# Kernel optimization log

Hardware: AMD Instinct MI355X
Metric: run time of the kernel (lower is better)

## Reference

```python
import jax, jax.numpy as jnp
import numpy as np

D_MODEL = 768
MIMO_RANK = 4


def setup_inputs() -> dict:
    key = jax.random.key(0)
    ks = jax.random.split(key, 6)
    B, T, D, R = 2, 2048, D_MODEL, MIMO_RANK
    x = jax.random.normal(ks[0], (B, T, D), dtype=jnp.float32)
    norm_w = jnp.ones((D,), dtype=jnp.float32)
    W_in = jax.random.normal(ks[1], (D * R * 2, D), dtype=jnp.float32) * 0.02
    W_out = jax.random.normal(ks[2], (D, D), dtype=jnp.float32) * 0.02
    a_param = jax.random.normal(ks[3], (D, R, 2), dtype=jnp.float32) * 0.12
    b_param = jax.random.normal(ks[4], (D, R, 2), dtype=jnp.float32) * 0.15
    c_param = jax.random.normal(ks[5], (D, R, 2), dtype=jnp.float32) * 0.15
    return {"x": x, "norm_w": norm_w, "W_in": W_in, "W_out": W_out,
            "a_param": a_param, "b_param": b_param, "c_param": c_param}


def reference(x, norm_w, W_in, W_out, a_param, b_param, c_param):
    B, T, D = x.shape
    R = a_param.shape[1]
    # RMSNorm
    xn = x * jax.lax.rsqrt(jnp.mean(x * x, axis=-1, keepdims=True) + 1e-6) * norm_w
    # in_proj -> interleaved complex MIMO input u: [B,T,D,R,2]
    u = (xn @ W_in.T).reshape(B, T, D, R, 2)
    # coefficients (tanh-bounded; |a| scaled by 0.97 for stability)
    a = jnp.tanh(a_param) * 0.97
    b = jnp.tanh(b_param)
    c = jnp.tanh(c_param)
    ac = jax.lax.complex(a[..., 0], a[..., 1])  # [D,R]
    bc = jax.lax.complex(b[..., 0], b[..., 1])
    cc = jax.lax.complex(c[..., 0], c[..., 1])
    uc = jax.lax.complex(u[..., 0], u[..., 1])  # [B,T,D,R]
    # linear complex recurrence s_t = a * s_{t-1} + b * u_t, zero init state,
    # parallelized with an associative scan over time.
    bu = bc[None, None] * uc
    A = jnp.broadcast_to(ac[None, None], bu.shape)

    def comb(l, r):
        return (l[0] * r[0], r[0] * l[1] + r[1])

    _, s = jax.lax.associative_scan(comb, (A, bu), axis=1)  # [B,T,D,R] complex
    # output mix: real part of c * h, summed over MIMO rank -> [B,T,D]
    y = jnp.real(cc[None, None] * s).sum(axis=-1)
    return y @ W_out.T
```

## Files before the change

kernel.cpp:

```cpp
#include <hip/hip_runtime.h>
#include <hip/hip_bf16.h>
#include <stdint.h>

#define BATCH 2
#define TT 2048
#define DM 768
#define RR 4
#define M_TOK 4096
#define NFEAT 6144
#define NCH 6144
#define CHUNK 64
#define NCHUNK 32

typedef __attribute__((ext_vector_type(8))) short short8;
typedef __attribute__((ext_vector_type(4))) float float4v;

__device__ inline float bf2f(uint32_t bits16) {
    union { uint32_t u; float f; } x; x.u = bits16 << 16; return x.f;
}

typedef const __attribute__((address_space(1))) void* gptr_t;
typedef __attribute__((address_space(3))) void* lptr_t;

__device__ inline void async_ld16(const void* g, void* l) {
    __builtin_amdgcn_global_load_lds((gptr_t)(uintptr_t)g, (lptr_t)(uintptr_t)l,
                                     16, 0, 0);
}

__device__ inline void store_c(__hip_bfloat16* C, size_t idx, float v) {
    C[idx] = __float2bfloat16(v);
}
__device__ inline void store_c(float* C, size_t idx, float v) { C[idx] = v; }

__global__ void prep_kernel(const float* __restrict__ W_in,
                            const float* __restrict__ W_out,
                            const float* __restrict__ ap,
                            const float* __restrict__ bp,
                            const float* __restrict__ cp,
                            __hip_bfloat16* __restrict__ Win_bf,
                            __hip_bfloat16* __restrict__ Wout_bf,
                            float2* __restrict__ ac, float2* __restrict__ bc,
                            float2* __restrict__ cc, float2* __restrict__ aL) {
    const int n1 = NFEAT * DM;
    const int n2 = DM * DM;
    int i = blockIdx.x * 256 + threadIdx.x;
    if (i < n1) Win_bf[i] = __float2bfloat16(W_in[i]);
    else if (i < n1 + n2) Wout_bf[i - n1] = __float2bfloat16(W_out[i - n1]);
    if (i < DM * RR) {
        float ar = tanhf(ap[2 * i])     * 0.97f;
        float ai = tanhf(ap[2 * i + 1]) * 0.97f;
        ac[i] = make_float2(ar, ai);
        bc[i] = make_float2(tanhf(bp[2 * i]), tanhf(bp[2 * i + 1]));
        cc[i] = make_float2(tanhf(cp[2 * i]), tanhf(cp[2 * i + 1]));
        float xr = ar, xi = ai;
        #pragma unroll
        for (int k = 0; k < 6; ++k) {
            float nr = xr * xr - xi * xi;
            float ni = 2.f * xr * xi;
            xr = nr; xi = ni;
        }
        aL[i] = make_float2(xr, xi);
    }
}

__global__ __launch_bounds__(256) void rmsnorm_kernel(
    const float* __restrict__ x, const float* __restrict__ w,
    __hip_bfloat16* __restrict__ xn) {
    int row = blockIdx.x;
    const float* xr = x + (size_t)row * DM;
    int tid = threadIdx.x;
    float v0 = xr[tid], v1 = xr[tid + 256], v2 = xr[tid + 512];
    float ss = v0 * v0 + v1 * v1 + v2 * v2;
    #pragma unroll
    for (int o = 1; o < 64; o <<= 1) ss += __shfl_xor(ss, o);
    __shared__ float wsum[4];
    if ((tid & 63) == 0) wsum[tid >> 6] = ss;
    __syncthreads();
    float tot = wsum[0] + wsum[1] + wsum[2] + wsum[3];
    float scale = rsqrtf(tot * (1.f / DM) + 1e-6f);
    size_t base = (size_t)row * DM;
    xn[base + tid]       = __float2bfloat16(v0 * scale * w[tid]);
    xn[base + tid + 256] = __float2bfloat16(v1 * scale * w[tid + 256]);
    xn[base + tid + 512] = __float2bfloat16(v2 * scale * w[tid + 512]);
}

template <int BM, int BN, typename OutT>
__global__ __launch_bounds__(256) void gemm_bt(
    const __hip_bfloat16* __restrict__ A, const __hip_bfloat16* __restrict__ B,
    OutT* __restrict__ C, int M, int N, int K) {
    constexpr int MI = BM / 32;
    constexpr int NJ = BN / 32;
    __shared__ __attribute__((aligned(16))) __hip_bfloat16 lA[BM * 64];
    __shared__ __attribute__((aligned(16))) __hip_bfloat16 lB[BN * 64];
    const int tid  = threadIdx.x;
    const int lane = tid & 63;
    const int wave = tid >> 6;
    const int quad = lane >> 4;
    const int l15  = lane & 15;
    const int wm = (wave >> 1) * (BM / 2);
    const int wn = (wave & 1) * (BN / 2);
    const int m0 = blockIdx.y * BM;
    const int n0 = blockIdx.x * BN;

    float4v acc[MI][NJ] = {};

    for (int k0 = 0; k0 < K; k0 += 64) {
        __syncthreads();
        #pragma unroll
        for (int it = 0; it < BM / 32; ++it) {
            int p = it * 256 + tid;
            int row = p >> 3;
            int cg = (p & 7) ^ (row & 7);
            async_ld16(A + (size_t)(m0 + row) * K + k0 + cg * 8, lA + p * 8);
        }
        #pragma unroll
        for (int it = 0; it < BN / 32; ++it) {
            int p = it * 256 + tid;
            int row = p >> 3;
            int cg = (p & 7) ^ (row & 7);
            async_ld16(B + (size_t)(n0 + row) * K + k0 + cg * 8, lB + p * 8);
        }
        __syncthreads();
        #pragma unroll
        for (int s = 0; s < 2; ++s) {
            short8 af[MI], bfr[NJ];
            #pragma unroll
            for (int i = 0; i < MI; ++i) {
                int r = wm + i * 16 + l15;
                int c = (s * 4 + quad) ^ (r & 7);
                af[i] = *(const short8*)(lA + r * 64 + c * 8);
            }
            #pragma unroll
            for (int j = 0; j < NJ; ++j) {
                int r = wn + j * 16 + l15;
                int c = (s * 4 + quad) ^ (r & 7);
                bfr[j] = *(const short8*)(lB + r * 64 + c * 8);
            }
            #pragma unroll
            for (int i = 0; i < MI; ++i)
                #pragma unroll
                for (int j = 0; j < NJ; ++j)
                    acc[i][j] = __builtin_amdgcn_mfma_f32_16x16x32_bf16(
                        af[i], bfr[j], acc[i][j], 0, 0, 0);
        }
    }
    #pragma unroll
    for (int i = 0; i < MI; ++i)
        #pragma unroll
        for (int j = 0; j < NJ; ++j)
            #pragma unroll
            for (int rg = 0; rg < 4; ++rg) {
                int row = m0 + wm + i * 16 + quad * 4 + rg;
                int col = n0 + wn + j * 16 + l15;
                store_c(C, (size_t)row * N + col, acc[i][j][rg]);
            }
}

__global__ __launch_bounds__(256) void scan_passA(
    const uint32_t* __restrict__ u,
    const float2* __restrict__ ac, const float2* __restrict__ bc,
    float2* __restrict__ chunkEnd) {
    int c = blockIdx.x * 256 + threadIdx.x;
    int j = blockIdx.y;
    int b = c >= DM * RR;
    int rem = c - b * DM * RR;
    float2 a = ac[rem], bb = bc[rem];
    float sr = 0.f, si = 0.f;
    size_t base = ((size_t)b * TT + (size_t)j * CHUNK) * (DM * RR) + rem;
    #pragma unroll 8
    for (int i = 0; i < CHUNK; ++i) {
        uint32_t uw = u[base + (size_t)i * (DM * RR)];
        float ur = bf2f(uw & 0xffffu), ui = bf2f(uw >> 16);
        float tr = bb.x * ur - bb.y * ui;
        float ti = bb.x * ui + bb.y * ur;
        float nr = a.x * sr - a.y * si + tr;
        float ni = a.x * si + a.y * sr + ti;
        sr = nr; si = ni;
    }
    chunkEnd[(size_t)j * NCH + c] = make_float2(sr, si);
}

__global__ __launch_bounds__(256) void scan_passC(
    const uint32_t* __restrict__ u,
    const float2* __restrict__ ac, const float2* __restrict__ bc,
    const float2* __restrict__ cc, const float2* __restrict__ aLp,
    const float2* __restrict__ chunkEnd,
    __hip_bfloat16* __restrict__ y) {
    int c = blockIdx.x * 256 + threadIdx.x;
    int j = blockIdx.y;
    int b = c >= DM * RR;
    int rem = c - b * DM * RR;
    int d = rem >> 2;
    float2 a = ac[rem], bb = bc[rem], cf = cc[rem];
    float2 aL = aLp[rem];
    float sr = 0.f, si = 0.f;
    #pragma unroll 4
    for (int jj = 0; jj < j; ++jj) {
        float2 e = chunkEnd[(size_t)jj * NCH + c];
        float nr = aL.x * sr - aL.y * si + e.x;
        float ni = aL.x * si + aL.y * sr + e.y;
        sr = nr; si = ni;
    }
    size_t ubase = ((size_t)b * TT + (size_t)j * CHUNK) * (DM * RR) + rem;
    size_t ybase = ((size_t)b * TT + (size_t)j * CHUNK) * DM + d;
    #pragma unroll 4
    for (int i = 0; i < CHUNK; ++i) {
        uint32_t uw = u[ubase + (size_t)i * (DM * RR)];
        float ur = bf2f(uw & 0xffffu), ui = bf2f(uw >> 16);
        float tr = bb.x * ur - bb.y * ui;
        float ti = bb.x * ui + bb.y * ur;
        float nr = a.x * sr - a.y * si + tr;
        float ni = a.x * si + a.y * sr + ti;
        sr = nr; si = ni;
        float contrib = cf.x * sr - cf.y * si;
        contrib += __shfl_xor(contrib, 1);
        contrib += __shfl_xor(contrib, 2);
        if ((threadIdx.x & 3) == 0)
            y[ybase + (size_t)i * DM] = __float2bfloat16(contrib);
    }
}

extern "C" void kernel_launch(void* const* d_in, const int* in_sizes, int n_in,
                              void* d_out, int out_size, void* d_ws,
                              size_t ws_size, hipStream_t stream) {
    const float* x      = (const float*)d_in[0];
    const float* norm_w = (const float*)d_in[1];
    const float* W_in   = (const float*)d_in[2];
    const float* W_out  = (const float*)d_in[3];
    const float* a_p    = (const float*)d_in[4];
    const float* b_p    = (const float*)d_in[5];
    const float* c_p    = (const float*)d_in[6];
    float* out = (float*)d_out;

    char* ws = (char*)d_ws;
    size_t off = 0;
    auto alloc = [&](size_t bytes) {
        void* p = ws + off;
        off += (bytes + 255) & ~(size_t)255;
        return p;
    };
    __hip_bfloat16* Win_bf  = (__hip_bfloat16*)alloc((size_t)NFEAT * DM * 2);
    __hip_bfloat16* Wout_bf = (__hip_bfloat16*)alloc((size_t)DM * DM * 2);
    __hip_bfloat16* xn      = (__hip_bfloat16*)alloc((size_t)M_TOK * DM * 2);
    __hip_bfloat16* u       = (__hip_bfloat16*)alloc((size_t)M_TOK * NFEAT * 2);
    __hip_bfloat16* y       = (__hip_bfloat16*)alloc((size_t)M_TOK * DM * 2);
    float2* ac = (float2*)alloc((size_t)DM * RR * 8);
    float2* bc = (float2*)alloc((size_t)DM * RR * 8);
    float2* cc = (float2*)alloc((size_t)DM * RR * 8);
    float2* aL = (float2*)alloc((size_t)DM * RR * 8);
    float2* chunkEnd = (float2*)alloc((size_t)NCHUNK * NCH * 8);

    {
        int n_total = NFEAT * DM + DM * DM;
        prep_kernel<<<(n_total + 255) / 256, 256, 0, stream>>>(
            W_in, W_out, a_p, b_p, c_p, Win_bf, Wout_bf, ac, bc, cc, aL);
    }
    rmsnorm_kernel<<<M_TOK, 256, 0, stream>>>(x, norm_w, xn);
    gemm_bt<128, 128, __hip_bfloat16>
        <<<dim3(NFEAT / 128, M_TOK / 128), 256, 0, stream>>>(
            xn, Win_bf, u, M_TOK, NFEAT, DM);
    scan_passA<<<dim3(NCH / 256, NCHUNK), 256, 0, stream>>>(
        (const uint32_t*)u, ac, bc, chunkEnd);
    scan_passC<<<dim3(NCH / 256, NCHUNK), 256, 0, stream>>>(
        (const uint32_t*)u, ac, bc, cc, aL, chunkEnd, y);
    gemm_bt<64, 64, float>
        <<<dim3(DM / 64, M_TOK / 64), 256, 0, stream>>>(
            y, Wout_bf, out, M_TOK, DM, DM);
}
```

Baseline: 192.7 us.

## Vectorize prep/rmsnorm, per-channel scan with rank-4 threads, add carry pass, BK=128 out-GEMM

The weight conversion and RMSNorm now use float4 loads and packed bf16 stores. The scan kernels assign one thread per model channel, handling all four MIMO ranks through a single 16-byte load, which removes the shuffle reduction in the output pass. A new passB computes the inter-chunk carries once, replacing the per-block serial prefix that every passC block used to recompute. The output GEMM uses a BK of 128. In exchange there is one extra kernel launch and a carry buffer, and the scan now launches 4x fewer threads, which lowers parallelism.

```diff
diff --git a/kernel.cpp b/kernel.cpp
--- a/kernel.cpp
+++ b/kernel.cpp
@@ -32,20 +32,31 @@
 }
 __device__ inline void store_c(float* C, size_t idx, float v) { C[idx] = v; }
 
-__global__ void prep_kernel(const float* __restrict__ W_in,
-                            const float* __restrict__ W_out,
-                            const float* __restrict__ ap,
-                            const float* __restrict__ bp,
-                            const float* __restrict__ cp,
-                            __hip_bfloat16* __restrict__ Win_bf,
-                            __hip_bfloat16* __restrict__ Wout_bf,
-                            float2* __restrict__ ac, float2* __restrict__ bc,
-                            float2* __restrict__ cc, float2* __restrict__ aL) {
-    const int n1 = NFEAT * DM;
-    const int n2 = DM * DM;
+__device__ inline uint2 pack4bf(float a, float b, float c, float d) {
+    union { __hip_bfloat16 h[4]; uint2 u; } o;
+    o.h[0] = __float2bfloat16(a); o.h[1] = __float2bfloat16(b);
+    o.h[2] = __float2bfloat16(c); o.h[3] = __float2bfloat16(d);
+    return o.u;
+}
+
+__global__ __launch_bounds__(256) void prep_kernel(
+    const float* __restrict__ W_in, const float* __restrict__ W_out,
+    const float* __restrict__ ap, const float* __restrict__ bp,
+    const float* __restrict__ cp,
+    __hip_bfloat16* __restrict__ Win_bf, __hip_bfloat16* __restrict__ Wout_bf,
+    float2* __restrict__ ac, float2* __restrict__ bc,
+    float2* __restrict__ cc, float2* __restrict__ aL) {
+    const int N1 = NFEAT * DM / 4;
+    const int N2 = DM * DM / 4;
     int i = blockIdx.x * 256 + threadIdx.x;
-    if (i < n1) Win_bf[i] = __float2bfloat16(W_in[i]);
-    else if (i < n1 + n2) Wout_bf[i - n1] = __float2bfloat16(W_out[i - n1]);
+    if (i < N1) {
+        float4 v = ((const float4*)W_in)[i];
+        ((uint2*)Win_bf)[i] = pack4bf(v.x, v.y, v.z, v.w);
+    } else if (i < N1 + N2) {
+        int k = i - N1;
+        float4 v = ((const float4*)W_out)[k];
+        ((uint2*)Wout_bf)[k] = pack4bf(v.x, v.y, v.z, v.w);
+    }
     if (i < DM * RR) {
         float ar = tanhf(ap[2 * i])     * 0.97f;
         float ai = tanhf(ap[2 * i + 1]) * 0.97f;
@@ -63,35 +74,35 @@
     }
 }
 
-__global__ __launch_bounds__(256) void rmsnorm_kernel(
+__global__ __launch_bounds__(192) void rmsnorm_kernel(
     const float* __restrict__ x, const float* __restrict__ w,
     __hip_bfloat16* __restrict__ xn) {
     int row = blockIdx.x;
-    const float* xr = x + (size_t)row * DM;
     int tid = threadIdx.x;
-    float v0 = xr[tid], v1 = xr[tid + 256], v2 = xr[tid + 512];
-    float ss = v0 * v0 + v1 * v1 + v2 * v2;
+    float4 v = ((const float4*)(x + (size_t)row * DM))[tid];
+    float ss = v.x * v.x + v.y * v.y + v.z * v.z + v.w * v.w;
     #pragma unroll
     for (int o = 1; o < 64; o <<= 1) ss += __shfl_xor(ss, o);
-    __shared__ float wsum[4];
+    __shared__ float wsum[3];
     if ((tid & 63) == 0) wsum[tid >> 6] = ss;
     __syncthreads();
-    float tot = wsum[0] + wsum[1] + wsum[2] + wsum[3];
+    float tot = wsum[0] + wsum[1] + wsum[2];
     float scale = rsqrtf(tot * (1.f / DM) + 1e-6f);
-    size_t base = (size_t)row * DM;
-    xn[base + tid]       = __float2bfloat16(v0 * scale * w[tid]);
-    xn[base + tid + 256] = __float2bfloat16(v1 * scale * w[tid + 256]);
-    xn[base + tid + 512] = __float2bfloat16(v2 * scale * w[tid + 512]);
-}
-
-template <int BM, int BN, typename OutT>
-__global__ __launch_bounds__(256) void gemm_bt(
+    float4 wv = ((const float4*)w)[tid];
+    ((uint2*)(xn + (size_t)row * DM))[tid] =
+        pack4bf(v.x * scale * wv.x, v.y * scale * wv.y,
+                v.z * scale * wv.z, v.w * scale * wv.w);
+}
+
+template <int BM, int BN, int BK, typename OutT>
+__device__ inline void gemm_body(
     const __hip_bfloat16* __restrict__ A, const __hip_bfloat16* __restrict__ B,
     OutT* __restrict__ C, int M, int N, int K) {
     constexpr int MI = BM / 32;
     constexpr int NJ = BN / 32;
-    __shared__ __attribute__((aligned(16))) __hip_bfloat16 lA[BM * 64];
-    __shared__ __attribute__((aligned(16))) __hip_bfloat16 lB[BN * 64];
+    constexpr int CPR = BK / 8;
+    __shared__ __attribute__((aligned(16))) __hip_bfloat16 lA[BM * BK];
+    __shared__ __attribute__((aligned(16))) __hip_bfloat16 lB[BN * BK];
     const int tid  = threadIdx.x;
     const int lane = tid & 63;
     const int wave = tid >> 6;
@@ -104,37 +115,37 @@
 
     float4v acc[MI][NJ] = {};
 
-    for (int k0 = 0; k0 < K; k0 += 64) {
+    for (int k0 = 0; k0 < K; k0 += BK) {
         __syncthreads();
         #pragma unroll
-        for (int it = 0; it < BM / 32; ++it) {
+        for (int it = 0; it < BM * CPR / 256; ++it) {
             int p = it * 256 + tid;
-            int row = p >> 3;
-            int cg = (p & 7) ^ (row & 7);
+            int row = p / CPR;
+            int cg = (p & (CPR - 1)) ^ (row & (CPR - 1));
             async_ld16(A + (size_t)(m0 + row) * K + k0 + cg * 8, lA + p * 8);
         }
         #pragma unroll
-        for (int it = 0; it < BN / 32; ++it) {
+        for (int it = 0; it < BN * CPR / 256; ++it) {
             int p = it * 256 + tid;
-            int row = p >> 3;
-            int cg = (p & 7) ^ (row & 7);
+            int row = p / CPR;
+            int cg = (p & (CPR - 1)) ^ (row & (CPR - 1));
             async_ld16(B + (size_t)(n0 + row) * K + k0 + cg * 8, lB + p * 8);
         }
         __syncthreads();
         #pragma unroll
-        for (int s = 0; s < 2; ++s) {
+        for (int s = 0; s < BK / 32; ++s) {
             short8 af[MI], bfr[NJ];
             #pragma unroll
             for (int i = 0; i < MI; ++i) {
                 int r = wm + i * 16 + l15;
-                int c = (s * 4 + quad) ^ (r & 7);
-                af[i] = *(const short8*)(lA + r * 64 + c * 8);
+                int c = (s * 4 + quad) ^ (r & (CPR - 1));
+                af[i] = *(const short8*)(lA + r * BK + c * 8);
             }
             #pragma unroll
             for (int j = 0; j < NJ; ++j) {
                 int r = wn + j * 16 + l15;
-                int c = (s * 4 + quad) ^ (r & 7);
-                bfr[j] = *(const short8*)(lB + r * 64 + c * 8);
+                int c = (s * 4 + quad) ^ (r & (CPR - 1));
+                bfr[j] = *(const short8*)(lB + r * BK + c * 8);
             }
             #pragma unroll
             for (int i = 0; i < MI; ++i)
@@ -156,67 +167,102 @@
             }
 }
 
+__global__ __launch_bounds__(256) void gemm_in(
+    const __hip_bfloat16* __restrict__ A, const __hip_bfloat16* __restrict__ B,
+    __hip_bfloat16* __restrict__ C, int M, int N, int K) {
+    gemm_body<128, 128, 64, __hip_bfloat16>(A, B, C, M, N, K);
+}
+
+__global__ __launch_bounds__(256) void gemm_out(
+    const __hip_bfloat16* __restrict__ A, const __hip_bfloat16* __restrict__ B,
+    float* __restrict__ C, int M, int N, int K) {
+    gemm_body<64, 64, 128, float>(A, B, C, M, N, K);
+}
+
+__device__ inline void cstep(float& sr, float& si, float2 a, float2 bb,
+                             uint32_t uw) {
+    float ur = bf2f(uw & 0xffffu), ui = bf2f(uw >> 16);
+    float tr = bb.x * ur - bb.y * ui;
+    float ti = bb.x * ui + bb.y * ur;
+    float nr = a.x * sr - a.y * si + tr;
+    float ni = a.x * si + a.y * sr + ti;
+    sr = nr; si = ni;
+}
+
 __global__ __launch_bounds__(256) void scan_passA(
-    const uint32_t* __restrict__ u,
+    const uint4* __restrict__ u4,
     const float2* __restrict__ ac, const float2* __restrict__ bc,
     float2* __restrict__ chunkEnd) {
+    int g = blockIdx.x * 256 + threadIdx.x;
+    int j = blockIdx.y;
+    int b = g >= DM;
+    int d = g - b * DM;
+    int cb = d * RR;
+    float2 a0 = ac[cb], a1 = ac[cb + 1], a2 = ac[cb + 2], a3 = ac[cb + 3];
+    float2 b0 = bc[cb], b1 = bc[cb + 1], b2 = bc[cb + 2], b3 = bc[cb + 3];
+    float s0r = 0, s0i = 0, s1r = 0, s1i = 0;
+    float s2r = 0, s2i = 0, s3r = 0, s3i = 0;
+    size_t base = ((size_t)(b * TT + j * CHUNK)) * DM + d;
+    #pragma unroll 4
+    for (int i = 0; i < CHUNK; ++i) {
+        uint4 uw = u4[base + (size_t)i * DM];
+        cstep(s0r, s0i, a0, b0, uw.x);
+        cstep(s1r, s1i, a1, b1, uw.y);
+        cstep(s2r, s2i, a2, b2, uw.z);
+        cstep(s3r, s3i, a3, b3, uw.w);
+    }
+    size_t eb = (size_t)j * NCH + b * (DM * RR) + cb;
+    chunkEnd[eb]     = make_float2(s0r, s0i);
+    chunkEnd[eb + 1] = make_float2(s1r, s1i);
+    chunkEnd[eb + 2] = make_float2(s2r, s2i);
+    chunkEnd[eb + 3] = make_float2(s3r, s3i);
+}
+
+__global__ __launch_bounds__(256) void scan_passB(
+    const float2* __restrict__ chunkEnd, const float2* __restrict__ aLp,
+    float2* __restrict__ carry) {
     int c = blockIdx.x * 256 + threadIdx.x;
-    int j = blockIdx.y;
-    int b = c >= DM * RR;
-    int rem = c - b * DM * RR;
-    float2 a = ac[rem], bb = bc[rem];
-    float sr = 0.f, si = 0.f;
-    size_t base = ((size_t)b * TT + (size_t)j * CHUNK) * (DM * RR) + rem;
-    #pragma unroll 8
-    for (int i = 0; i < CHUNK; ++i) {
-        uint32_t uw = u[base + (size_t)i * (DM * RR)];
-        float ur = bf2f(uw & 0xffffu), ui = bf2f(uw >> 16);
-        float tr = bb.x * ur - bb.y * ui;
-        float ti = bb.x * ui + bb.y * ur;
-        float nr = a.x * sr - a.y * si + tr;
-        float ni = a.x * si + a.y * sr + ti;
-        sr = nr; si = ni;
-    }
-    chunkEnd[(size_t)j * NCH + c] = make_float2(sr, si);
-}
-
-__global__ __launch_bounds__(256) void scan_passC(
-    const uint32_t* __restrict__ u,
-    const float2* __restrict__ ac, const float2* __restrict__ bc,
-    const float2* __restrict__ cc, const float2* __restrict__ aLp,
-    const float2* __restrict__ chunkEnd,
-    __hip_bfloat16* __restrict__ y) {
-    int c = blockIdx.x * 256 + threadIdx.x;
-    int j = blockIdx.y;
-    int b = c >= DM * RR;
-    int rem = c - b * DM * RR;
-    int d = rem >> 2;
-    float2 a = ac[rem], bb = bc[rem], cf = cc[rem];
+    int rem = (c >= DM * RR) ? c - DM * RR : c;
     float2 aL = aLp[rem];
     float sr = 0.f, si = 0.f;
-    #pragma unroll 4
-    for (int jj = 0; jj < j; ++jj) {
-        float2 e = chunkEnd[(size_t)jj * NCH + c];
+    for (int j = 0; j < NCHUNK; ++j) {
+        carry[(size_t)j * NCH + c] = make_float2(sr, si);
+        float2 e = chunkEnd[(size_t)j * NCH + c];
         float nr = aL.x * sr - aL.y * si + e.x;
         float ni = aL.x * si + aL.y * sr + e.y;
         sr = nr; si = ni;
     }
-    size_t ubase = ((size_t)b * TT + (size_t)j * CHUNK) * (DM * RR) + rem;
-    size_t ybase = ((size_t)b * TT + (size_t)j * CHUNK) * DM + d;
+}
+
+__global__ __launch_bounds__(256) void scan_passC(
+    const uint4* __restrict__ u4,
+    const float2* __restrict__ ac, const float2* __restrict__ bc,
+    const float2* __restrict__ cc, const float2* __restrict__ carry,
+    __hip_bfloat16* __restrict__ y) {
+    int g = blockIdx.x * 256 + threadIdx.x;
+    int j = blockIdx.y;
+    int b = g >= DM;
+    int d = g - b * DM;
+    int cb = d * RR;
+    float2 a0 = ac[cb], a1 = ac[cb + 1], a2 = ac[cb + 2], a3 = ac[cb + 3];
+    float2 b0 = bc[cb], b1 = bc[cb + 1], b2 = bc[cb + 2], b3 = bc[cb + 3];
+    float2 c0 = cc[cb], c1 = cc[cb + 1], c2 = cc[cb + 2], c3 = cc[cb + 3];
+    size_t kb = (size_t)j * NCH + b * (DM * RR) + cb;
+    float2 k0 = carry[kb], k1 = carry[kb + 1];
+    float2 k2 = carry[kb + 2], k3 = carry[kb + 3];
+    float s0r = k0.x, s0i = k0.y, s1r = k1.x, s1i = k1.y;
+    float s2r = k2.x, s2i = k2.y, s3r = k3.x, s3i = k3.y;
+    size_t base  = ((size_t)(b * TT + j * CHUNK)) * DM + d;
     #pragma unroll 4
     for (int i = 0; i < CHUNK; ++i) {
-        uint32_t uw = u[ubase + (size_t)i * (DM * RR)];
-        float ur = bf2f(uw & 0xffffu), ui = bf2f(uw >> 16);
-        float tr = bb.x * ur - bb.y * ui;
-        float ti = bb.x * ui + bb.y * ur;
-        float nr = a.x * sr - a.y * si + tr;
-        float ni = a.x * si + a.y * sr + ti;
-        sr = nr; si = ni;
-        float contrib = cf.x * sr - cf.y * si;
-        contrib += __shfl_xor(contrib, 1);
-        contrib += __shfl_xor(contrib, 2);
-        if ((threadIdx.x & 3) == 0)
-            y[ybase + (size_t)i * DM] = __float2bfloat16(contrib);
+        uint4 uw = u4[base + (size_t)i * DM];
+        cstep(s0r, s0i, a0, b0, uw.x);
+        cstep(s1r, s1i, a1, b1, uw.y);
+        cstep(s2r, s2i, a2, b2, uw.z);
+        cstep(s3r, s3i, a3, b3, uw.w);
+        float yv = c0.x * s0r - c0.y * s0i + c1.x * s1r - c1.y * s1i
+                 + c2.x * s2r - c2.y * s2i + c3.x * s3r - c3.y * s3i;
+        y[base + (size_t)i * DM] = __float2bfloat16(yv);
     }
 }
 
@@ -249,21 +295,21 @@
     float2* cc = (float2*)alloc((size_t)DM * RR * 8);
     float2* aL = (float2*)alloc((size_t)DM * RR * 8);
     float2* chunkEnd = (float2*)alloc((size_t)NCHUNK * NCH * 8);
+    float2* carry    = (float2*)alloc((size_t)NCHUNK * NCH * 8);
 
     {
-        int n_total = NFEAT * DM + DM * DM;
+        int n_total = (NFEAT * DM + DM * DM) / 4;
         prep_kernel<<<(n_total + 255) / 256, 256, 0, stream>>>(
             W_in, W_out, a_p, b_p, c_p, Win_bf, Wout_bf, ac, bc, cc, aL);
     }
-    rmsnorm_kernel<<<M_TOK, 256, 0, stream>>>(x, norm_w, xn);
-    gemm_bt<128, 128, __hip_bfloat16>
-        <<<dim3(NFEAT / 128, M_TOK / 128), 256, 0, stream>>>(
-            xn, Win_bf, u, M_TOK, NFEAT, DM);
-    scan_passA<<<dim3(NCH / 256, NCHUNK), 256, 0, stream>>>(
-        (const uint32_t*)u, ac, bc, chunkEnd);
-    scan_passC<<<dim3(NCH / 256, NCHUNK), 256, 0, stream>>>(
-        (const uint32_t*)u, ac, bc, cc, aL, chunkEnd, y);
-    gemm_bt<64, 64, float>
-        <<<dim3(DM / 64, M_TOK / 64), 256, 0, stream>>>(
-            y, Wout_bf, out, M_TOK, DM, DM);
-}
+    rmsnorm_kernel<<<M_TOK, 192, 0, stream>>>(x, norm_w, xn);
+    gemm_in<<<dim3(NFEAT / 128, M_TOK / 128), 256, 0, stream>>>(
+        xn, Win_bf, u, M_TOK, NFEAT, DM);
+    scan_passA<<<dim3(BATCH * DM / 256, NCHUNK), 256, 0, stream>>>(
+        (const uint4*)u, ac, bc, chunkEnd);
+    scan_passB<<<NCH / 256, 256, 0, stream>>>(chunkEnd, aL, carry);
+    scan_passC<<<dim3(BATCH * DM / 256, NCHUNK), 256, 0, stream>>>(
+        (const uint4*)u, ac, bc, cc, carry, y);
+    gemm_out<<<dim3(DM / 64, M_TOK / 64), 256, 0, stream>>>(
+        y, Wout_bf, out, M_TOK, DM, DM);
+}
```

Result: no change. 192.7 us (-0.0%).
